# Optimization experiments

Measured on AMD Instinct MI355X. Metric: run time of the kernel, lower is better.

Reference implementation:

```python
import jax, jax.numpy as jnp
import numpy as np

LOG2PI = float(np.log(2.0 * np.pi))
MIN_DURATION = 1
NUM_STATES = 512
OBS_DIM = 128
B, T, K = 64, 2000, 400


def setup_inputs() -> dict:
    key = jax.random.key(0)
    ks = jax.random.split(key, 10)
    observations = jax.random.normal(ks[0], (B, T, OBS_DIM), dtype=jnp.float32)
    state_sequence = jax.random.randint(ks[1], (B, K), 0, NUM_STATES, dtype=jnp.int32)
    # durations >= min_duration so gamma log-prob stays finite
    duration_sequence = jax.random.randint(ks[2], (B, K), 1, 51, dtype=jnp.int32)
    # learned parameters, initialized as in the torch module
    alpha_params = jnp.ones((NUM_STATES,), jnp.float32)
    beta_params = jnp.ones((NUM_STATES,), jnp.float32)
    transition_logits = jax.random.normal(ks[3], (NUM_STATES, NUM_STATES), dtype=jnp.float32)
    initial_logits = jnp.zeros((NUM_STATES,), jnp.float32)
    observation_means = jax.random.normal(ks[4], (NUM_STATES, OBS_DIM), dtype=jnp.float32)
    observation_logvars = jnp.zeros((NUM_STATES, OBS_DIM), jnp.float32)
    return {
        "observations": observations,
        "alpha_params": alpha_params,
        "beta_params": beta_params,
        "transition_logits": transition_logits,
        "initial_logits": initial_logits,
        "observation_means": observation_means,
        "observation_logvars": observation_logvars,
        "state_sequence": state_sequence,
        "duration_sequence": duration_sequence,
    }


def _gamma_duration_logprob(alpha_params, beta_params, state_sequence, duration_sequence):
    # fully vectorized version of the per-sample Python loop in DurationModel
    d = duration_sequence.astype(jnp.float32)                      # [B, K]
    alpha = jax.nn.softplus(alpha_params)[state_sequence] + 1e-6   # [B, K]
    beta = jax.nn.softplus(beta_params)[state_sequence] + 1e-6
    lp = (alpha - 1.0) * jnp.log(d + 1e-8) - beta * d
    lp = lp - (jax.lax.lgamma(alpha) - alpha * jnp.log(beta))
    return jnp.where(d >= MIN_DURATION, lp, -jnp.inf)


def reference(observations, alpha_params, beta_params, transition_logits,
              initial_logits, observation_means, observation_logvars,
              state_sequence, duration_sequence):
    # --- duration log-probs per segment: [B, K]
    log_dur = _gamma_duration_logprob(alpha_params, beta_params,
                                      state_sequence, duration_sequence)

    # --- expand segments to frames: frame t belongs to segment with cum[idx-1] <= t < cum[idx]
    cum = jnp.cumsum(duration_sequence, axis=1)                    # [B, K]
    t = jnp.arange(observations.shape[1])                          # [T]
    seg_idx = jax.vmap(lambda c: jnp.searchsorted(c, t, side='right'))(cum)
    seg_idx = jnp.clip(seg_idx, 0, state_sequence.shape[1] - 1)    # [B, T]
    frame_states = jnp.take_along_axis(state_sequence, seg_idx, axis=1)  # [B, T]

    # --- diagonal-gaussian observation log-probs per frame: [B, T]
    mu = observation_means[frame_states]                           # [B, T, D]
    lv = observation_logvars[frame_states]                         # [B, T, D]
    resid2 = (observations - mu) ** 2 * jnp.exp(-lv)
    log_obs = -0.5 * jnp.sum(lv + resid2 + LOG2PI, axis=-1)        # [B, T]

    # --- initial + transition log-probs over the segment-level state chain
    log_trans = jax.nn.log_softmax(transition_logits, axis=-1)     # [S, S]
    log_init = jax.nn.log_softmax(initial_logits)                  # [S]
    trans_lp = log_trans[state_sequence[:, :-1], state_sequence[:, 1:]].sum(axis=1)  # [B]
    init_lp = log_init[state_sequence[:, 0]]                       # [B]

    # --- per-sequence supervised log-likelihood: [B]
    log_likelihood = log_obs.sum(axis=1) + log_dur.sum(axis=1) + trans_lp + init_lp
    return log_likelihood
```

## Files before the change

### kernel.cpp

```cpp
#include <hip/hip_runtime.h>
#include <hip/hip_bf16.h>
#include <math.h>

#define NS 512
#define OD 128
#define BB 64
#define TT 2000
#define KK 400
#define CHUNK 128
#define NCH 16
#define LOG2PI_F 1.8378770664093453f
#define PART_OFF 4096


__device__ __forceinline__ float softplusf(float x) {
    return (x > 20.f) ? x : log1pf(expf(x));
}

__global__ __launch_bounds__(256) void big_kernel(
    const float* __restrict__ obs, const float* __restrict__ mu,
    const float* __restrict__ lvar, const float* __restrict__ trans,
    const float* __restrict__ init_logits,
    const int* __restrict__ states, const int* __restrict__ durs,
    float* __restrict__ ws)
{
    const int tid = threadIdx.x;
    const int bid = blockIdx.x;
    __shared__ float red[4];

    if (bid < BB * NCH) {
        const int b = bid >> 4;
        const int chunk = bid & 15;
        const int t0 = chunk * CHUNK;

        __shared__ int st[KK];
        __shared__ int cum[512];
        __shared__ int fsl[CHUNK];

        for (int k = tid; k < KK; k += 256) {
            st[k]  = states[b * KK + k];
            cum[k] = durs[b * KK + k];
        }
        for (int k = KK + tid; k < 512; k += 256) cum[k] = 0;
        __syncthreads();
        for (int off = 1; off < 512; off <<= 1) {
            const int i0 = tid, i1 = tid + 256;
            int v0 = (i0 >= off) ? cum[i0 - off] : 0;
            int v1 = (i1 >= off) ? cum[i1 - off] : 0;
            __syncthreads();
            cum[i0] += v0;
            cum[i1] += v1;
            __syncthreads();
        }
        for (int k = KK + tid; k < 512; k += 256) cum[k] = 0x7fffffff;
        __syncthreads();
        if (tid < CHUNK) {
            const int t = t0 + tid;
            int lo = 0, hi = 512;
            while (lo < hi) {
                int mid = (lo + hi) >> 1;
                if (cum[mid] <= t) lo = mid + 1; else hi = mid;
            }
            fsl[tid] = st[(lo > KK - 1) ? (KK - 1) : lo];
        }
        __syncthreads();

        const int row = tid >> 5;
        const int d = (tid & 31) * 4;
        float acc = 0.f;
        #pragma unroll
        for (int i = 0; i < CHUNK / 8; ++i) {
            const int t = t0 + i * 8 + row;
            if (t < TT) {
                const int s = fsl[i * 8 + row];
                const float4 o  = *(const float4*)(obs + ((size_t)(b * TT + t)) * OD + d);
                const float4 m  = *(const float4*)(mu  + (size_t)s * OD + d);
                const float4 lv = *(const float4*)(lvar + (size_t)s * OD + d);
                const float dx = o.x - m.x, dy = o.y - m.y, dz = o.z - m.z, dw = o.w - m.w;
                acc += lv.x + lv.y + lv.z + lv.w + 4.f * LOG2PI_F
                     + dx * dx * __expf(-lv.x) + dy * dy * __expf(-lv.y)
                     + dz * dz * __expf(-lv.z) + dw * dw * __expf(-lv.w);
            }
        }
        for (int off = 32; off; off >>= 1) acc += __shfl_down(acc, off, 64);
        if ((tid & 63) == 0) red[tid >> 6] = acc;
        __syncthreads();
        if (tid == 0)
            ws[PART_OFF + bid] = red[0] + red[1] + red[2] + red[3];
    } else {
        const int r = bid - BB * NCH;
        const float* src = (r < NS) ? (trans + (size_t)r * NS) : init_logits;
        float x0 = src[tid];
        float x1 = src[tid + 256];
        float m = fmaxf(x0, x1);
        for (int off = 32; off; off >>= 1) m = fmaxf(m, __shfl_down(m, off, 64));
        if ((tid & 63) == 0) red[tid >> 6] = m;
        __syncthreads();
        m = fmaxf(fmaxf(red[0], red[1]), fmaxf(red[2], red[3]));
        __syncthreads();
        float e = __expf(x0 - m) + __expf(x1 - m);
        for (int off = 32; off; off >>= 1) e += __shfl_down(e, off, 64);
        if ((tid & 63) == 0) red[tid >> 6] = e;
        __syncthreads();
        if (tid == 0) {
            float lse = m + __logf(red[0] + red[1] + red[2] + red[3]);
            ws[(r < NS) ? r : 512] = lse;
        }
    }
}

__global__ __launch_bounds__(256) void fin_kernel(
    const float* __restrict__ alpha_p, const float* __restrict__ beta_p,
    const float* __restrict__ trans, const float* __restrict__ init_logits,
    const int* __restrict__ states, const int* __restrict__ durs,
    const float* __restrict__ ws, float* __restrict__ out)
{
    const int b = blockIdx.x;
    const int tid = threadIdx.x;
    __shared__ float red[4];

    float lp = 0.f;
    if (tid < NCH) lp = -0.5f * ws[PART_OFF + b * NCH + tid];

    for (int k = tid; k < KK; k += 256) {
        const int s = states[b * KK + k];
        const float dv = (float)durs[b * KK + k];
        const float a  = softplusf(alpha_p[s]) + 1e-6f;
        const float bt = softplusf(beta_p[s]) + 1e-6f;
        float v = (a - 1.f) * __logf(dv + 1e-8f) - bt * dv + a * __logf(bt) - lgammaf(a);
        lp += (dv >= 1.f) ? v : -INFINITY;
        if (k < KK - 1)
            lp += trans[(size_t)s * NS + states[b * KK + k + 1]] - ws[s];
    }
    for (int off = 32; off; off >>= 1) lp += __shfl_down(lp, off, 64);
    if ((tid & 63) == 0) red[tid >> 6] = lp;
    __syncthreads();
    if (tid == 0)
        out[b] = red[0] + red[1] + red[2] + red[3]
               + init_logits[states[b * KK]] - ws[512];
}

extern "C" void kernel_launch(void* const* d_in, const int* in_sizes, int n_in,
                              void* d_out, int out_size, void* d_ws, size_t ws_size,
                              hipStream_t stream) {
    const float* observations = (const float*)d_in[0];
    const float* alpha_p      = (const float*)d_in[1];
    const float* beta_p       = (const float*)d_in[2];
    const float* trans        = (const float*)d_in[3];
    const float* init_logits  = (const float*)d_in[4];
    const float* obs_means    = (const float*)d_in[5];
    const float* obs_logvars  = (const float*)d_in[6];
    const int*   state_seq    = (const int*)d_in[7];
    const int*   dur_seq      = (const int*)d_in[8];

    float* ws = (float*)d_ws;
    float* out = (float*)d_out;

    big_kernel<<<BB * NCH + NS + 1, 256, 0, stream>>>(
        observations, obs_means, obs_logvars, trans, init_logits,
        state_seq, dur_seq, ws);
    fin_kernel<<<BB, 256, 0, stream>>>(
        alpha_p, beta_p, trans, init_logits, state_seq, dur_seq, ws, out);
}
```

Measured before the change: 26.02 us.

## Use wave-shuffle prefix scan and move duration/transition terms into the main kernel

Replaces the shared-memory Hillis-Steele scan over durations, which needed about 18 block barriers, with a wave-level shuffle scan plus a small cross-wave offset pass. The binary search now runs only over the 400 valid entries. The per-sequence duration log-prob and transition gathers move into 64 extra blocks of the first kernel, so they run alongside the observation work. The final kernel then only subtracts the log-sum-exp terms and adds the partials, which shortens the serial tail but adds another workspace region.

New measurement: 22.21 us. 14.6% less time.

```diff
diff --git a/kernel.cpp b/kernel.cpp
--- a/kernel.cpp
+++ b/kernel.cpp
@@ -11,6 +11,7 @@
 #define NCH 16
 #define LOG2PI_F 1.8378770664093453f
 #define PART_OFF 4096
+#define SEQ_OFF  5632
 
 
 __device__ __forceinline__ float softplusf(float x) {
@@ -21,6 +22,7 @@
     const float* __restrict__ obs, const float* __restrict__ mu,
     const float* __restrict__ lvar, const float* __restrict__ trans,
     const float* __restrict__ init_logits,
+    const float* __restrict__ alpha_p, const float* __restrict__ beta_p,
     const int* __restrict__ states, const int* __restrict__ durs,
     float* __restrict__ ws)
 {
@@ -30,33 +32,40 @@
 
     if (bid < BB * NCH) {
         const int b = bid >> 4;
-        const int chunk = bid & 15;
-        const int t0 = chunk * CHUNK;
+        const int t0 = (bid & 15) * CHUNK;
 
         __shared__ int st[KK];
         __shared__ int cum[512];
+        __shared__ int csum[8];
         __shared__ int fsl[CHUNK];
 
-        for (int k = tid; k < KK; k += 256) {
-            st[k]  = states[b * KK + k];
-            cum[k] = durs[b * KK + k];
+        const int lane = tid & 63, w = tid >> 6;
+        int v0 = 0, v1 = 0;
+        if (tid < KK) { st[tid] = states[b * KK + tid]; v0 = durs[b * KK + tid]; }
+        if (tid + 256 < KK) { st[tid + 256] = states[b * KK + tid + 256];
+                              v1 = durs[b * KK + tid + 256]; }
+        #pragma unroll
+        for (int off = 1; off < 64; off <<= 1) {
+            int u0 = __shfl_up(v0, off, 64);
+            int u1 = __shfl_up(v1, off, 64);
+            if (lane >= off) { v0 += u0; v1 += u1; }
         }
-        for (int k = KK + tid; k < 512; k += 256) cum[k] = 0;
+        if (lane == 63) { csum[w] = v0; csum[4 + w] = v1; }
         __syncthreads();
-        for (int off = 1; off < 512; off <<= 1) {
-            const int i0 = tid, i1 = tid + 256;
-            int v0 = (i0 >= off) ? cum[i0 - off] : 0;
-            int v1 = (i1 >= off) ? cum[i1 - off] : 0;
-            __syncthreads();
-            cum[i0] += v0;
-            cum[i1] += v1;
-            __syncthreads();
+        int off0 = 0, off1 = 0;
+        #pragma unroll
+        for (int c = 0; c < 8; ++c) {
+            int cs = csum[c];
+            off0 += (c < w) ? cs : 0;
+            off1 += (c < 4 + w) ? cs : 0;
         }
-        for (int k = KK + tid; k < 512; k += 256) cum[k] = 0x7fffffff;
+        cum[tid] = v0 + off0;
+        cum[tid + 256] = v1 + off1;
         __syncthreads();
+
         if (tid < CHUNK) {
             const int t = t0 + tid;
-            int lo = 0, hi = 512;
+            int lo = 0, hi = KK;
             while (lo < hi) {
                 int mid = (lo + hi) >> 1;
                 if (cum[mid] <= t) lo = mid + 1; else hi = mid;
@@ -87,7 +96,7 @@
         __syncthreads();
         if (tid == 0)
             ws[PART_OFF + bid] = red[0] + red[1] + red[2] + red[3];
-    } else {
+    } else if (bid < BB * NCH + NS + 1) {
         const int r = bid - BB * NCH;
         const float* src = (r < NS) ? (trans + (size_t)r * NS) : init_logits;
         float x0 = src[tid];
@@ -102,17 +111,32 @@
         for (int off = 32; off; off >>= 1) e += __shfl_down(e, off, 64);
         if ((tid & 63) == 0) red[tid >> 6] = e;
         __syncthreads();
-        if (tid == 0) {
-            float lse = m + __logf(red[0] + red[1] + red[2] + red[3]);
-            ws[(r < NS) ? r : 512] = lse;
+        if (tid == 0)
+            ws[(r < NS) ? r : 512] = m + __logf(red[0] + red[1] + red[2] + red[3]);
+    } else {
+        const int b = bid - (BB * NCH + NS + 1);
+        float lp = 0.f;
+        for (int k = tid; k < KK; k += 256) {
+            const int s = states[b * KK + k];
+            const float dv = (float)durs[b * KK + k];
+            const float a  = softplusf(alpha_p[s]) + 1e-6f;
+            const float bt = softplusf(beta_p[s]) + 1e-6f;
+            float v = (a - 1.f) * __logf(dv + 1e-8f) - bt * dv
+                    + a * __logf(bt) - lgammaf(a);
+            lp += (dv >= 1.f) ? v : -INFINITY;
+            if (k < KK - 1)
+                lp += trans[(size_t)s * NS + states[b * KK + k + 1]];
         }
+        for (int off = 32; off; off >>= 1) lp += __shfl_down(lp, off, 64);
+        if ((tid & 63) == 0) red[tid >> 6] = lp;
+        __syncthreads();
+        if (tid == 0)
+            ws[SEQ_OFF + b] = red[0] + red[1] + red[2] + red[3];
     }
 }
 
 __global__ __launch_bounds__(256) void fin_kernel(
-    const float* __restrict__ alpha_p, const float* __restrict__ beta_p,
-    const float* __restrict__ trans, const float* __restrict__ init_logits,
-    const int* __restrict__ states, const int* __restrict__ durs,
+    const float* __restrict__ init_logits, const int* __restrict__ states,
     const float* __restrict__ ws, float* __restrict__ out)
 {
     const int b = blockIdx.x;
@@ -120,18 +144,10 @@
     __shared__ float red[4];
 
     float lp = 0.f;
-    if (tid < NCH) lp = -0.5f * ws[PART_OFF + b * NCH + tid];
-
-    for (int k = tid; k < KK; k += 256) {
-        const int s = states[b * KK + k];
-        const float dv = (float)durs[b * KK + k];
-        const float a  = softplusf(alpha_p[s]) + 1e-6f;
-        const float bt = softplusf(beta_p[s]) + 1e-6f;
-        float v = (a - 1.f) * __logf(dv + 1e-8f) - bt * dv + a * __logf(bt) - lgammaf(a);
-        lp += (dv >= 1.f) ? v : -INFINITY;
-        if (k < KK - 1)
-            lp += trans[(size_t)s * NS + states[b * KK + k + 1]] - ws[s];
-    }
+    if (tid < NCH)        lp = -0.5f * ws[PART_OFF + b * NCH + tid];
+    else if (tid == NCH)  lp = ws[SEQ_OFF + b];
+    for (int k = tid; k < KK - 1; k += 256)
+        lp -= ws[states[b * KK + k]];
     for (int off = 32; off; off >>= 1) lp += __shfl_down(lp, off, 64);
     if ((tid & 63) == 0) red[tid >> 6] = lp;
     __syncthreads();
@@ -156,9 +172,8 @@
     float* ws = (float*)d_ws;
     float* out = (float*)d_out;
 
-    big_kernel<<<BB * NCH + NS + 1, 256, 0, stream>>>(
+    big_kernel<<<BB * NCH + NS + 1 + BB, 256, 0, stream>>>(
         observations, obs_means, obs_logvars, trans, init_logits,
-        state_seq, dur_seq, ws);
-    fin_kernel<<<BB, 256, 0, stream>>>(
-        alpha_p, beta_p, trans, init_logits, state_seq, dur_seq, ws, out);
+        alpha_p, beta_p, state_seq, dur_seq, ws);
+    fin_kernel<<<BB, 256, 0, stream>>>(init_logits, state_seq, ws, out);
 }
```
